# Optimization experiments

Measured on AMD Instinct MI355X. Metric: run time of the kernel, lower is better.

Reference implementation:

```python
import jax, jax.numpy as jnp
import numpy as np

E = 2048      # embedding_size
H = 16        # num_heads
D = 128       # head_dim
G = 4         # gqa_factor
KH = H // G   # kv heads
F = 8192      # up_proj_size
B, S = 2, 2048


def _layer_norm(x, g, b, eps=1e-5):
    mu = jnp.mean(x, axis=-1, keepdims=True)
    var = jnp.mean(jnp.square(x - mu), axis=-1, keepdims=True)
    return (x - mu) * jax.lax.rsqrt(var + eps) * g + b


def setup_inputs() -> dict:
    key = jax.random.key(0)
    ks = jax.random.split(key, 16)
    std = 0.02
    inp = {
        'x': jax.random.normal(ks[0], (B, S, E), dtype=jnp.float32),
        'ln1_g': jnp.ones((E,), jnp.float32),
        'ln1_b': jnp.zeros((E,), jnp.float32),
        'wq': jax.random.normal(ks[1], (E, H * D), jnp.float32) * std,
        'bq': jnp.zeros((H * D,), jnp.float32),
        'wk': jax.random.normal(ks[2], (E, KH * D), jnp.float32) * std,
        'bk': jnp.zeros((KH * D,), jnp.float32),
        'wv': jax.random.normal(ks[3], (E, KH * D), jnp.float32) * std,
        'bv': jnp.zeros((KH * D,), jnp.float32),
        'wo': jax.random.normal(ks[4], (H * D, E), jnp.float32) * std,
        'bo': jnp.zeros((E,), jnp.float32),
        'ln2_g': jnp.ones((E,), jnp.float32),
        'ln2_b': jnp.zeros((E,), jnp.float32),
        'wu': jax.random.normal(ks[5], (E, F), jnp.float32) * std,
        'bu': jnp.zeros((F,), jnp.float32),
        'wd': jax.random.normal(ks[6], (F, E), jnp.float32) * std,
        'bd': jnp.zeros((E,), jnp.float32),
    }
    return inp


def _block(x, ln1_g, ln1_b, wq, bq, wk, bk, wv, bv, wo, bo, ln2_g, ln2_b, wu, bu, wd, bd):
    b, s, e = x.shape
    # attention sub-block (use_cache=False, train_mode=False -> no dropout)
    x1 = _layer_norm(x, ln1_g, ln1_b)
    q = (x1 @ wq + bq).reshape(b, s, H, D).transpose(0, 2, 1, 3)       # (B,H,S,D)
    q = q.reshape(b, KH, G, s, D)                                       # (B,KH,G,S,D)
    k = (x1 @ wk + bk).reshape(b, s, KH, D).transpose(0, 2, 1, 3)      # (B,KH,S,D)
    v = (x1 @ wv + bv).reshape(b, s, KH, D).transpose(0, 2, 1, 3)      # (B,KH,S,D)
    scores = jnp.einsum('bkgsd,bktd->bkgst', q, k) / np.sqrt(D).astype(np.float32)
    causal = jnp.tril(jnp.ones((s, s), dtype=bool))                     # True = keep
    scores = jnp.where(causal, scores, -jnp.inf)
    att = jax.nn.softmax(scores, axis=-1)
    o = jnp.einsum('bkgst,bktd->bkgsd', att, v)                         # (B,KH,G,S,D)
    o = o.reshape(b, H, s, D).transpose(0, 2, 1, 3).reshape(b, s, H * D)
    x = x + (o @ wo + bo)
    # MLP sub-block
    x2 = _layer_norm(x, ln2_g, ln2_b)
    h = jax.nn.gelu(x2 @ wu + bu, approximate=False)
    x = x + (h @ wd + bd)
    return x


def reference(x, ln1_g, ln1_b, wq, bq, wk, bk, wv, bv, wo, bo, ln2_g, ln2_b, wu, bu, wd, bd):
    return _block(x, ln1_g, ln1_b, wq, bq, wk, bk, wv, bv, wo, bo, ln2_g, ln2_b, wu, bu, wd, bd)
```

## Files before the change

### kernel.cpp

```cpp
#include <hip/hip_runtime.h>
#include <hip/hip_bf16.h>
#include <cstdint>
#include <math.h>

typedef unsigned short u16;
using f32x4   = __attribute__((ext_vector_type(4))) float;
using short8  = __attribute__((ext_vector_type(8))) short;
using short4v = __attribute__((ext_vector_type(4))) short;

#define DEV static __device__ __forceinline__

DEV u16 f2bf(float f) {
  union { float f; unsigned u; } v; v.f = f;
  unsigned r = v.u + 0x7fffu + ((v.u >> 16) & 1u);
  return (u16)(r >> 16);
}

DEV f32x4 mfma_bf16(short8 a, short8 b, f32x4 c) {
  return __builtin_amdgcn_mfma_f32_16x16x32_bf16(a, b, c, 0, 0, 0);
}

DEV void gload16(const void* g, void* l) {
  __builtin_amdgcn_global_load_lds((const __attribute__((address_space(1))) void*)g,
                                   (__attribute__((address_space(3))) void*)l,
                                   16, 0, 0);
}

__global__ __launch_bounds__(256) void transpose_cvt(
    const float* __restrict__ in, u16* __restrict__ out, int K, int N)
{
  __shared__ float tile[32][33];
  const int n0 = blockIdx.x * 32, k0 = blockIdx.y * 32;
  const int c = threadIdx.x & 31, r = threadIdx.x >> 5;
#pragma unroll
  for (int i = 0; i < 4; i++) {
    const int row = r + i * 8;
    tile[row][c] = in[(size_t)(k0 + row) * N + n0 + c];
  }
  __syncthreads();
#pragma unroll
  for (int i = 0; i < 4; i++) {
    const int row = r + i * 8;
    out[(size_t)(n0 + row) * K + k0 + c] = f2bf(tile[c][row]);
  }
}

__global__ __launch_bounds__(256) void ln_kernel(
    const float* __restrict__ x, const float* __restrict__ g,
    const float* __restrict__ bt, u16* __restrict__ out)
{
  __shared__ float red1[4], red2[4];
  const int row = blockIdx.x;
  const int t = threadIdx.x;
  const int lane = t & 63, w = t >> 6;
  const float* xr = x + (size_t)row * 2048 + t * 8;
  float v[8];
  {
    const float4* p4 = (const float4*)xr;
    float4 a = p4[0], b = p4[1];
    v[0] = a.x; v[1] = a.y; v[2] = a.z; v[3] = a.w;
    v[4] = b.x; v[5] = b.y; v[6] = b.z; v[7] = b.w;
  }
  float s = 0.f;
#pragma unroll
  for (int j = 0; j < 8; j++) s += v[j];
#pragma unroll
  for (int m = 1; m < 64; m <<= 1) s += __shfl_xor(s, m);
  if (lane == 0) red1[w] = s;
  __syncthreads();
  const float mu = (red1[0] + red1[1] + red1[2] + red1[3]) * (1.f / 2048.f);
  float q = 0.f;
#pragma unroll
  for (int j = 0; j < 8; j++) { v[j] -= mu; q += v[j] * v[j]; }
#pragma unroll
  for (int m = 1; m < 64; m <<= 1) q += __shfl_xor(q, m);
  if (lane == 0) red2[w] = q;
  __syncthreads();
  const float rstd = rsqrtf((red2[0] + red2[1] + red2[2] + red2[3]) * (1.f / 2048.f) + 1e-5f);
  const float4* g4 = (const float4*)(g + t * 8);
  const float4* b4 = (const float4*)(bt + t * 8);
  float4 ga = g4[0], gb = g4[1], ba = b4[0], bb = b4[1];
  float gg[8] = {ga.x, ga.y, ga.z, ga.w, gb.x, gb.y, gb.z, gb.w};
  float bbv[8] = {ba.x, ba.y, ba.z, ba.w, bb.x, bb.y, bb.z, bb.w};
  short8 o;
#pragma unroll
  for (int j = 0; j < 8; j++) o[j] = (short)f2bf(v[j] * rstd * gg[j] + bbv[j]);
  *(short8*)&out[(size_t)row * 2048 + t * 8] = o;
}

template<int MODE, int N, int K>
__global__ void __launch_bounds__(256) gemm_bt(
    const u16* __restrict__ A, const u16* __restrict__ Bt,
    const float* __restrict__ bias,
    u16* __restrict__ out_bf)
{
  __shared__ u16 As[128 * 64];
  __shared__ u16 Bs[128 * 64];
  const int m0 = blockIdx.y * 128;
  const int n0 = blockIdx.x * 128;
  const int tid = threadIdx.x;
  const int lane = tid & 63, w = tid >> 6;
  const int wm = w >> 1, wn = w & 1;
  const int z = lane >> 4, l15 = lane & 15;

  f32x4 acc[4][4];
#pragma unroll
  for (int m = 0; m < 4; m++)
#pragma unroll
    for (int n = 0; n < 4; n++)
#pragma unroll
      for (int i = 0; i < 4; i++) acc[m][n][i] = 0.f;

  for (int k0 = 0; k0 < K; k0 += 64) {
#pragma unroll
    for (int j = 0; j < 4; j++) {
      const int seg = w * 4 + j;
      const int c = seg * 64 + lane;
      const int r = c >> 3;
      const int cc = (c & 7) ^ (r & 7);
      gload16(A + (size_t)(m0 + r) * K + k0 + cc * 8, &As[seg * 512]);
    }
#pragma unroll
    for (int j = 0; j < 4; j++) {
      const int seg = w * 4 + j;
      const int c = seg * 64 + lane;
      const int r = c >> 3;
      const int cc = (c & 7) ^ (r & 7);
      gload16(Bt + (size_t)(n0 + r) * K + k0 + cc * 8, &Bs[seg * 512]);
    }
    asm volatile("s_waitcnt vmcnt(0)" ::: "memory");
    __syncthreads();

#pragma unroll
    for (int kk = 0; kk < 2; kk++) {
      short8 af[4], bfr[4];
#pragma unroll
      for (int m = 0; m < 4; m++) {
        const int row = wm * 64 + m * 16 + l15;
        const int off = row * 64 + ((kk * 32 + z * 8) ^ ((row & 7) << 3));
        af[m] = *(const short8*)&As[off];
      }
#pragma unroll
      for (int n = 0; n < 4; n++) {
        const int row = wn * 64 + n * 16 + l15;
        const int off = row * 64 + ((kk * 32 + z * 8) ^ ((row & 7) << 3));
        bfr[n] = *(const short8*)&Bs[off];
      }
#pragma unroll
      for (int m = 0; m < 4; m++)
#pragma unroll
        for (int n = 0; n < 4; n++)
          acc[m][n] = mfma_bf16(af[m], bfr[n], acc[m][n]);
    }
    __syncthreads();
  }

#pragma unroll
  for (int m = 0; m < 4; m++) {
    const int row0 = m0 + wm * 64 + m * 16 + z * 4;
#pragma unroll
    for (int n = 0; n < 4; n++) {
      const int col = n0 + wn * 64 + n * 16 + l15;
      f32x4 v = acc[m][n];
      const float bb = bias[col];
      if constexpr (MODE == 1) {
#pragma unroll
        for (int i = 0; i < 4; i++)
          out_bf[(size_t)(row0 + i) * N + col] = f2bf(v[i] + bb);
      } else {
        const int bidx = row0 >> 11, sidx = row0 & 2047;
        const int kh = col >> 7, d = col & 127;
        short4v p;
#pragma unroll
        for (int i = 0; i < 4; i++) p[i] = (short)f2bf(v[i] + bb);
        *(short4v*)&out_bf[(size_t)((bidx * 4 + kh) * 128 + d) * 2048 + sidx] = p;
      }
    }
  }
}

template<int MODE, int BM, int N, int K>
__global__ void __launch_bounds__(512) gemm256(
    const u16* __restrict__ A, const u16* __restrict__ Bt,
    const float* __restrict__ bias, const float* __restrict__ resid,
    u16* __restrict__ out_bf, float* __restrict__ out_f)
{
  constexpr int BN = 256;
  constexpr int MREP = BM / 32;
  constexpr int LA = BM / 128;
  constexpr int L = LA + 2;
  constexpr int NT = K / 64;
  constexpr int NWG = (4096 / BM) * (N / BN);
  constexpr int CPX = NWG / 8;

  __shared__ u16 Al[2][2][BM * 32];
  __shared__ u16 Bl[2][2][BN * 32];

  const int bid = blockIdx.x;
  const int wg = (bid & 7) * CPX + (bid >> 3);
  const int bm = wg / (N / BN), bn = wg % (N / BN);
  const int m0 = bm * BM, n0 = bn * BN;
  const int tid = threadIdx.x, lane = tid & 63, w = tid >> 6;
  const int wm = w >> 2, wn = w & 3;
  const int z = lane >> 4, l15 = lane & 15;

  f32x4 acc[MREP][4];
#pragma unroll
  for (int m = 0; m < MREP; m++)
#pragma unroll
    for (int n = 0; n < 4; n++)
#pragma unroll
      for (int i = 0; i < 4; i++) acc[m][n][i] = 0.f;

  auto stage = [&](int tt, int kh) {
    const int buf = tt & 1;
    const int kc = tt * 64 + kh * 32;
#pragma unroll
    for (int j = 0; j < LA; j++) {
      const int gl = (w * LA + j) * 64 + lane;
      const int r = gl >> 2, gg = gl & 3;
      const int cg = gg ^ ((r >> 1) & 3);
      gload16(A + (size_t)(m0 + r) * K + kc + cg * 8, &Al[buf][kh][(w * LA + j) * 512]);
    }
#pragma unroll
    for (int j = 0; j < 2; j++) {
      const int gl = (w * 2 + j) * 64 + lane;
      const int r = gl >> 2, gg = gl & 3;
      const int cg = gg ^ ((r >> 1) & 3);
      gload16(Bt + (size_t)(n0 + r) * K + kc + cg * 8, &Bl[buf][kh][(w * 2 + j) * 512]);
    }
  };

  stage(0, 0); stage(0, 1); stage(1, 0); stage(1, 1);

  for (int t = 0; t < NT; t++) {
    const int cb = t & 1;
#pragma unroll
    for (int kh = 0; kh < 2; kh++) {
      if constexpr (L == 4) asm volatile("s_waitcnt vmcnt(4)" ::: "memory");
      else                  asm volatile("s_waitcnt vmcnt(3)" ::: "memory");
      __builtin_amdgcn_s_barrier();
      if (t + 1 < NT) stage(t + 1, kh);

      short8 af[MREP], bf[4];
#pragma unroll
      for (int m = 0; m < MREP; m++) {
        const int r = wm * (BM / 2) + m * 16 + l15;
        af[m] = *(const short8*)&Al[cb][kh][r * 32 + ((z ^ ((r >> 1) & 3)) * 8)];
      }
#pragma unroll
      for (int n = 0; n < 4; n++) {
        const int r = wn * 64 + n * 16 + l15;
        bf[n] = *(const short8*)&Bl[cb][kh][r * 32 + ((z ^ ((r >> 1) & 3)) * 8)];
      }
      __builtin_amdgcn_s_setprio(1);
#pragma unroll
      for (int m = 0; m < MREP; m++)
#pragma unroll
        for (int n = 0; n < 4; n++)
          acc[m][n] = mfma_bf16(af[m], bf[n], acc[m][n]);
      __builtin_amdgcn_s_setprio(0);
    }
  }

#pragma unroll
  for (int m = 0; m < MREP; m++) {
    const int row0 = m0 + wm * (BM / 2) + m * 16 + z * 4;
#pragma unroll
    for (int n = 0; n < 4; n++) {
      const int col = n0 + wn * 64 + n * 16 + l15;
      f32x4 v = acc[m][n];
      const float bb = bias[col];
      if constexpr (MODE == 0) {
#pragma unroll
        for (int i = 0; i < 4; i++)
          out_bf[(size_t)(row0 + i) * N + col] = f2bf((v[i] + bb) * 0.08838834764831845f);
      } else if constexpr (MODE == 3) {
#pragma unroll
        for (int i = 0; i < 4; i++) {
          const size_t idx = (size_t)(row0 + i) * N + col;
          out_f[idx] = v[i] + bb + resid[idx];
        }
      } else if constexpr (MODE == 4) {
#pragma unroll
        for (int i = 0; i < 4; i++) {
          const float xx = v[i] + bb;
          out_bf[(size_t)(row0 + i) * N + col] =
              f2bf(0.5f * xx * (1.f + erff(xx * 0.70710678118654752f)));
        }
      } else {
#pragma unroll
        for (int i = 0; i < 4; i++) {
          const size_t idx = (size_t)(row0 + i) * N + col;
          out_f[idx] = v[i] + bb + out_f[idx];
        }
      }
    }
  }
}

__global__ void __launch_bounds__(256) attn_kernel(
    const u16* __restrict__ qb, const u16* __restrict__ kb,
    const u16* __restrict__ vt, u16* __restrict__ ob)
{
  __shared__ u16 Kt[2][64 * 128];
  __shared__ u16 Vs[2][128 * 64];
  __shared__ u16 Pl[4 * 32 * 64];

  const int idx = blockIdx.x;
  const int xcd = idx & 7;
  const int u = (idx >> 3) & 31;
  const int half = idx >> 8;
  const int bh = xcd * 4 + (u & 3);
  const int qh = u >> 2;
  const int qt = half ? (15 - qh) : qh;

  const int b = bh >> 4, h = bh & 15, kh = h >> 2;
  const int q0 = qt * 128;
  const int tid = threadIdx.x, lane = tid & 63, w = tid >> 6;
  const int z = lane >> 4, l15 = lane & 15;
  const int qw0 = q0 + w * 32;
  const int ksw = (l15 & 7) << 3;

  short8 qf[2][4];
#pragma unroll
  for (int m = 0; m < 2; m++)
#pragma unroll
    for (int kk = 0; kk < 4; kk++)
      qf[m][kk] = *(const short8*)&qb[(size_t)(b * 2048 + qw0 + m * 16 + l15) * 2048 +
                                      h * 128 + kk * 32 + z * 8];

  f32x4 oacc[2][8];
#pragma unroll
  for (int m = 0; m < 2; m++)
#pragma unroll
    for (int n = 0; n < 8; n++)
#pragma unroll
      for (int i = 0; i < 4; i++) oacc[m][n][i] = 0.f;
  float mst[2][4], lst[2][4];
#pragma unroll
  for (int m = 0; m < 2; m++)
#pragma unroll
    for (int i = 0; i < 4; i++) { mst[m][i] = -1e30f; lst[m][i] = 0.f; }

  auto STAGE = [&](int tt, int bufsel) {
    const int kv0s = tt * 64;
#pragma unroll
    for (int j = 0; j < 4; j++) {
      const int seg = w * 4 + j;
      const int c = seg * 64 + lane;
      const int r = c >> 4;
      const int cc = (c & 15) ^ (r & 7);
      gload16(kb + (size_t)(b * 2048 + kv0s + r) * 512 + kh * 128 + cc * 8,
              &Kt[bufsel][seg * 512]);
    }
#pragma unroll
    for (int j = 0; j < 4; j++) {
      const int seg = w * 4 + j;
      const int c = seg * 64 + lane;
      const int d = c >> 3;
      const int cc = (c & 7) ^ (d & 7);
      gload16(vt + (size_t)((b * 4 + kh) * 128 + d) * 2048 + kv0s + cc * 8,
              &Vs[bufsel][seg * 512]);
    }
  };

  const int ntiles = q0 / 64 + 2;

  STAGE(0, 0);
  asm volatile("s_waitcnt vmcnt(0)" ::: "memory");
  __syncthreads();

  for (int t = 0; t < ntiles; t++) {
    const int cur = t & 1;
    if (t + 1 < ntiles) STAGE(t + 1, cur ^ 1);

    const int kv0 = t * 64;
    if (kv0 <= qw0 + 31) {
      f32x4 sf[2][4];
#pragma unroll
      for (int m = 0; m < 2; m++)
#pragma unroll
        for (int n = 0; n < 4; n++)
#pragma unroll
          for (int i = 0; i < 4; i++) sf[m][n][i] = 0.f;

      __builtin_amdgcn_s_setprio(1);
#pragma unroll
      for (int kk = 0; kk < 4; kk++) {
        short8 kfr[4];
#pragma unroll
        for (int n = 0; n < 4; n++) {
          const int row = n * 16 + l15;
          kfr[n] = *(const short8*)&Kt[cur][row * 128 + ((kk * 32 + z * 8) ^ ksw)];
        }
#pragma unroll
        for (int m = 0; m < 2; m++)
#pragma unroll
          for (int n = 0; n < 4; n++)
            sf[m][n] = mfma_bf16(qf[m][kk], kfr[n], sf[m][n]);
      }
      __builtin_amdgcn_s_setprio(0);

      u16* Pw = &Pl[w * 2048];
      const bool edge = (kv0 + 63 > qw0);
#pragma unroll
      for (int m = 0; m < 2; m++) {
#pragma unroll
        for (int i = 0; i < 4; i++) {
          const int rq = qw0 + m * 16 + z * 4 + i;
          if (edge) {
#pragma unroll
            for (int n = 0; n < 4; n++)
              if (kv0 + n * 16 + l15 > rq) sf[m][n][i] = -1e30f;
          }
          float mx = fmaxf(fmaxf(sf[m][0][i], sf[m][1][i]), fmaxf(sf[m][2][i], sf[m][3][i]));
          mx = fmaxf(mx, __shfl_xor(mx, 1));
          mx = fmaxf(mx, __shfl_xor(mx, 2));
          mx = fmaxf(mx, __shfl_xor(mx, 4));
          mx = fmaxf(mx, __shfl_xor(mx, 8));
          const bool grow = mx > mst[m][i];
          const float mn = grow ? mx : mst[m][i];
          float rs = 0.f;
#pragma unroll
          for (int n = 0; n < 4; n++) {
            const float p = __expf(sf[m][n][i] - mn);
            sf[m][n][i] = p;
            rs += p;
          }
          rs += __shfl_xor(rs, 1);
          rs += __shfl_xor(rs, 2);
          rs += __shfl_xor(rs, 4);
          rs += __shfl_xor(rs, 8);
          if (grow) {
            const float al = __expf(mst[m][i] - mx);
            mst[m][i] = mx;
            lst[m][i] = lst[m][i] * al + rs;
#pragma unroll
            for (int n = 0; n < 8; n++) oacc[m][n][i] *= al;
          } else {
            lst[m][i] += rs;
          }
          const int prow = m * 16 + z * 4 + i;
          const int psw = ((z * 4 + i) & 7) << 3;
#pragma unroll
          for (int n = 0; n < 4; n++)
            Pw[prow * 64 + ((n * 16 + l15) ^ psw)] = f2bf(sf[m][n][i]);
        }
      }

      __builtin_amdgcn_s_setprio(1);
#pragma unroll
      for (int kk = 0; kk < 2; kk++) {
        short8 af[2], vf[8];
#pragma unroll
        for (int m = 0; m < 2; m++) {
          const int row = m * 16 + l15;
          af[m] = *(const short8*)&Pw[row * 64 + ((kk * 32 + z * 8) ^ ksw)];
        }
#pragma unroll
        for (int n = 0; n < 8; n++) {
          const int row = n * 16 + l15;
          vf[n] = *(const short8*)&Vs[cur][row * 64 + ((kk * 32 + z * 8) ^ ksw)];
        }
#pragma unroll
        for (int m = 0; m < 2; m++)
#pragma unroll
          for (int n = 0; n < 8; n++)
            oacc[m][n] = mfma_bf16(af[m], vf[n], oacc[m][n]);
      }
      __builtin_amdgcn_s_setprio(0);
    }

    asm volatile("s_waitcnt vmcnt(0)" ::: "memory");
    __syncthreads();
  }

#pragma unroll
  for (int m = 0; m < 2; m++)
#pragma unroll
    for (int i = 0; i < 4; i++) {
      const float inv = 1.0f / lst[m][i];
      const int rq = qw0 + m * 16 + z * 4 + i;
      u16* orow = &ob[(size_t)(b * 2048 + rq) * 2048 + h * 128];
#pragma unroll
      for (int n = 0; n < 8; n++)
        orow[n * 16 + l15] = f2bf(oacc[m][n][i] * inv);
    }
}

extern "C" void kernel_launch(void* const* d_in, const int* in_sizes, int n_in,
                              void* d_out, int out_size, void* d_ws, size_t ws_size,
                              hipStream_t stream) {
  (void)in_sizes; (void)n_in; (void)out_size; (void)ws_size;
  const float* x     = (const float*)d_in[0];
  const float* ln1_g = (const float*)d_in[1];
  const float* ln1_b = (const float*)d_in[2];
  const float* wq    = (const float*)d_in[3];
  const float* bq    = (const float*)d_in[4];
  const float* wk    = (const float*)d_in[5];
  const float* bk    = (const float*)d_in[6];
  const float* wv    = (const float*)d_in[7];
  const float* bv    = (const float*)d_in[8];
  const float* wo    = (const float*)d_in[9];
  const float* bo    = (const float*)d_in[10];
  const float* ln2_g = (const float*)d_in[11];
  const float* ln2_b = (const float*)d_in[12];
  const float* wu    = (const float*)d_in[13];
  const float* bu    = (const float*)d_in[14];
  const float* wd    = (const float*)d_in[15];
  const float* bd    = (const float*)d_in[16];
  float* out = (float*)d_out;

  char* p = (char*)d_ws;
  u16* wqT = (u16*)p; p += (size_t)2048 * 2048 * 2;
  u16* wkT = (u16*)p; p += (size_t)512 * 2048 * 2;
  u16* wvT = (u16*)p; p += (size_t)512 * 2048 * 2;
  u16* woT = (u16*)p; p += (size_t)2048 * 2048 * 2;
  u16* wuT = (u16*)p; p += (size_t)8192 * 2048 * 2;
  u16* wdT = (u16*)p; p += (size_t)2048 * 8192 * 2;
  u16* x1  = (u16*)p; p += (size_t)4096 * 2048 * 2;
  u16* qbuf= (u16*)p; p += (size_t)4096 * 2048 * 2;
  u16* kbuf= (u16*)p; p += (size_t)4096 * 512 * 2;
  u16* vtb = (u16*)p; p += (size_t)4096 * 512 * 2;
  u16* hb  = (u16*)p; p += (size_t)4096 * 8192 * 2;
  u16* ob  = x1;
  u16* x2  = qbuf;

  transpose_cvt<<<dim3(64, 64),  256, 0, stream>>>(wq, wqT, 2048, 2048);
  transpose_cvt<<<dim3(16, 64),  256, 0, stream>>>(wk, wkT, 2048, 512);
  transpose_cvt<<<dim3(16, 64),  256, 0, stream>>>(wv, wvT, 2048, 512);
  transpose_cvt<<<dim3(64, 64),  256, 0, stream>>>(wo, woT, 2048, 2048);
  transpose_cvt<<<dim3(256, 64), 256, 0, stream>>>(wu, wuT, 2048, 8192);
  transpose_cvt<<<dim3(64, 256), 256, 0, stream>>>(wd, wdT, 8192, 2048);

  ln_kernel<<<4096, 256, 0, stream>>>(x, ln1_g, ln1_b, x1);

  gemm256<0, 128, 2048, 2048><<<256, 512, 0, stream>>>(x1, wqT, bq, nullptr, qbuf, nullptr);
  gemm_bt<1, 512, 2048><<<dim3(4, 32), 256, 0, stream>>>(x1, wkT, bk, kbuf);
  gemm_bt<2, 512, 2048><<<dim3(4, 32), 256, 0, stream>>>(x1, wvT, bv, vtb);

  attn_kernel<<<512, 256, 0, stream>>>(qbuf, kbuf, vtb, ob);

  gemm256<3, 128, 2048, 2048><<<256, 512, 0, stream>>>(ob, woT, bo, x, nullptr, out);

  ln_kernel<<<4096, 256, 0, stream>>>(out, ln2_g, ln2_b, x2);

  gemm256<4, 256, 8192, 2048><<<512, 512, 0, stream>>>(x2, wuT, bu, nullptr, hb, nullptr);
  gemm256<5, 128, 2048, 8192><<<256, 512, 0, stream>>>(hb, wdT, bd, nullptr, nullptr, out);
}
```

Measured before the change: 836.9 us.

## Restructure GEMM mainloop into a 4-slot ring with 3-deep prefetch

Replaces the double-buffered two-half-tile pipeline in the shared GEMM kernel with a 4-slot ring of 32-wide K slices, issuing loads three phases ahead and waiting on per-phase vmcnt values. It also precomputes the swizzled LDS and global address offsets once per thread instead of per load. The goal is to hide more global-load latency and cut address arithmetic. In exchange it adds a second barrier per phase, and the same LDS footprint is now split into smaller slices.

```diff
diff --git a/kernel.cpp b/kernel.cpp
--- a/kernel.cpp
+++ b/kernel.cpp
@@ -188,13 +188,12 @@
   constexpr int BN = 256;
   constexpr int MREP = BM / 32;
   constexpr int LA = BM / 128;
-  constexpr int L = LA + 2;
-  constexpr int NT = K / 64;
+  constexpr int P = K / 32;
   constexpr int NWG = (4096 / BM) * (N / BN);
   constexpr int CPX = NWG / 8;
 
-  __shared__ u16 Al[2][2][BM * 32];
-  __shared__ u16 Bl[2][2][BN * 32];
+  __shared__ u16 Al[4][BM * 32];
+  __shared__ u16 Bl[4][BN * 32];
 
   const int bid = blockIdx.x;
   const int wg = (bid & 7) * CPX + (bid >> 3);
@@ -203,6 +202,11 @@
   const int tid = threadIdx.x, lane = tid & 63, w = tid >> 6;
   const int wm = w >> 2, wn = w & 3;
   const int z = lane >> 4, l15 = lane & 15;
+  const int wmBase = wm * (BM / 2);
+  const int wnBase = wn * 64;
+  const int koff = (z ^ ((l15 >> 1) & 3)) * 8;
+  const int col8 = ((lane & 3) ^ ((lane >> 3) & 3)) * 8;
+  const int srow = lane >> 2;
 
   f32x4 acc[MREP][4];
 #pragma unroll
@@ -212,63 +216,71 @@
 #pragma unroll
       for (int i = 0; i < 4; i++) acc[m][n][i] = 0.f;
 
-  auto stage = [&](int tt, int kh) {
-    const int buf = tt & 1;
-    const int kc = tt * 64 + kh * 32;
+  auto stage = [&](int g) {
+    const int sl = g & 3;
+    const int kc = g * 32;
 #pragma unroll
     for (int j = 0; j < LA; j++) {
-      const int gl = (w * LA + j) * 64 + lane;
-      const int r = gl >> 2, gg = gl & 3;
-      const int cg = gg ^ ((r >> 1) & 3);
-      gload16(A + (size_t)(m0 + r) * K + kc + cg * 8, &Al[buf][kh][(w * LA + j) * 512]);
+      const int sweep = w * LA + j;
+      gload16(A + (size_t)(m0 + sweep * 16 + srow) * K + kc + col8, &Al[sl][sweep * 512]);
     }
 #pragma unroll
     for (int j = 0; j < 2; j++) {
-      const int gl = (w * 2 + j) * 64 + lane;
-      const int r = gl >> 2, gg = gl & 3;
-      const int cg = gg ^ ((r >> 1) & 3);
-      gload16(Bt + (size_t)(n0 + r) * K + kc + cg * 8, &Bl[buf][kh][(w * 2 + j) * 512]);
+      const int sweep = w * 2 + j;
+      gload16(Bt + (size_t)(n0 + sweep * 16 + srow) * K + kc + col8, &Bl[sl][sweep * 512]);
     }
   };
 
-  stage(0, 0); stage(0, 1); stage(1, 0); stage(1, 1);
-
-  for (int t = 0; t < NT; t++) {
-    const int cb = t & 1;
-#pragma unroll
-    for (int kh = 0; kh < 2; kh++) {
-      if constexpr (L == 4) asm volatile("s_waitcnt vmcnt(4)" ::: "memory");
-      else                  asm volatile("s_waitcnt vmcnt(3)" ::: "memory");
-      __builtin_amdgcn_s_barrier();
-      if (t + 1 < NT) stage(t + 1, kh);
-
-      short8 af[MREP], bf[4];
-#pragma unroll
-      for (int m = 0; m < MREP; m++) {
-        const int r = wm * (BM / 2) + m * 16 + l15;
-        af[m] = *(const short8*)&Al[cb][kh][r * 32 + ((z ^ ((r >> 1) & 3)) * 8)];
-      }
-#pragma unroll
-      for (int n = 0; n < 4; n++) {
-        const int r = wn * 64 + n * 16 + l15;
-        bf[n] = *(const short8*)&Bl[cb][kh][r * 32 + ((z ^ ((r >> 1) & 3)) * 8)];
-      }
-      __builtin_amdgcn_s_setprio(1);
-#pragma unroll
-      for (int m = 0; m < MREP; m++)
-#pragma unroll
-        for (int n = 0; n < 4; n++)
-          acc[m][n] = mfma_bf16(af[m], bf[n], acc[m][n]);
-      __builtin_amdgcn_s_setprio(0);
-    }
-  }
+#define PHASE(pp, VMSTR, DOSTAGE)                                              \
+  do {                                                                         \
+    asm volatile("s_waitcnt " VMSTR ::: "memory");                             \
+    __builtin_amdgcn_s_barrier();                                              \
+    asm volatile("" ::: "memory");                                             \
+    if (DOSTAGE) stage((pp) + 3);                                              \
+    const int sl_ = (pp) & 3;                                                  \
+    const u16* Ab_ = &Al[sl_][0];                                              \
+    const u16* Bb_ = &Bl[sl_][0];                                              \
+    short8 af_[MREP], bf_[4];                                                  \
+    _Pragma("unroll")                                                          \
+    for (int m = 0; m < MREP; m++)                                             \
+      af_[m] = *(const short8*)&Ab_[(wmBase + m * 16 + l15) * 32 + koff];      \
+    _Pragma("unroll")                                                          \
+    for (int n = 0; n < 4; n++)                                                \
+      bf_[n] = *(const short8*)&Bb_[(wnBase + n * 16 + l15) * 32 + koff];      \
+    asm volatile("s_waitcnt lgkmcnt(0)" ::: "memory");                         \
+    __builtin_amdgcn_sched_barrier(0);                                         \
+    __builtin_amdgcn_s_setprio(1);                                             \
+    _Pragma("unroll")                                                          \
+    for (int m = 0; m < MREP; m++)                                             \
+      _Pragma("unroll")                                                        \
+      for (int n = 0; n < 4; n++)                                              \
+        acc[m][n] = mfma_bf16(af_[m], bf_[n], acc[m][n]);                      \
+    __builtin_amdgcn_s_setprio(0);                                             \
+    asm volatile("" ::: "memory");                                             \
+    __builtin_amdgcn_s_barrier();                                              \
+  } while (0)
+
+  stage(0); stage(1); stage(2);
+
+  if constexpr (LA == 2) {
+    for (int p = 0; p < P - 3; p++) PHASE(p, "vmcnt(8)", true);
+    PHASE(P - 3, "vmcnt(8)", false);
+    PHASE(P - 2, "vmcnt(4)", false);
+    PHASE(P - 1, "vmcnt(0)", false);
+  } else {
+    for (int p = 0; p < P - 3; p++) PHASE(p, "vmcnt(6)", true);
+    PHASE(P - 3, "vmcnt(6)", false);
+    PHASE(P - 2, "vmcnt(3)", false);
+    PHASE(P - 1, "vmcnt(0)", false);
+  }
+#undef PHASE
 
 #pragma unroll
   for (int m = 0; m < MREP; m++) {
-    const int row0 = m0 + wm * (BM / 2) + m * 16 + z * 4;
+    const int row0 = m0 + wmBase + m * 16 + z * 4;
 #pragma unroll
     for (int n = 0; n < 4; n++) {
-      const int col = n0 + wn * 64 + n * 16 + l15;
+      const int col = n0 + wnBase + n * 16 + l15;
       f32x4 v = acc[m][n];
       const float bb = bias[col];
       if constexpr (MODE == 0) {
```

Result: slower. 867.1 us (+3.6%).

## Replace 512-thread 256-wide GEMM with 128x128 double-buffered 256-thread kernel

Applied to the files above, without the earlier changes.

Swaps the large-tile gemm256 kernel (BM up to 256, BN 256, 8 waves, split-k-half staging with partial vmcnt waits) for a simpler 128x128 tile, 4-wave kernel. The new kernel double-buffers full 64-wide K slices and waits on all loads plus a block-wide sync each iteration. It also uses an XOR-8 LDS swizzle. The smaller tiles launch more workgroups and may raise occupancy, but they lower per-tile data reuse and drop the finer-grained load/compute overlap.

```diff
diff --git a/kernel.cpp b/kernel.cpp
--- a/kernel.cpp
+++ b/kernel.cpp
@@ -179,93 +179,95 @@
   }
 }
 
-template<int MODE, int BM, int N, int K>
-__global__ void __launch_bounds__(512) gemm256(
+template<int MODE, int N, int K>
+__global__ void __launch_bounds__(256) gemm_db(
     const u16* __restrict__ A, const u16* __restrict__ Bt,
     const float* __restrict__ bias, const float* __restrict__ resid,
     u16* __restrict__ out_bf, float* __restrict__ out_f)
 {
-  constexpr int BN = 256;
-  constexpr int MREP = BM / 32;
-  constexpr int LA = BM / 128;
-  constexpr int L = LA + 2;
+  __shared__ u16 As[2][128 * 64];
+  __shared__ u16 Bs[2][128 * 64];
+  constexpr int TN = N / 128;
+  constexpr int NWG = 32 * TN;
+  constexpr int CPX = NWG / 8;
   constexpr int NT = K / 64;
-  constexpr int NWG = (4096 / BM) * (N / BN);
-  constexpr int CPX = NWG / 8;
-
-  __shared__ u16 Al[2][2][BM * 32];
-  __shared__ u16 Bl[2][2][BN * 32];
 
   const int bid = blockIdx.x;
   const int wg = (bid & 7) * CPX + (bid >> 3);
-  const int bm = wg / (N / BN), bn = wg % (N / BN);
-  const int m0 = bm * BM, n0 = bn * BN;
-  const int tid = threadIdx.x, lane = tid & 63, w = tid >> 6;
-  const int wm = w >> 2, wn = w & 3;
+  const int m0 = (wg / TN) * 128;
+  const int n0 = (wg % TN) * 128;
+  const int tid = threadIdx.x;
+  const int lane = tid & 63, w = tid >> 6;
+  const int wm = w >> 1, wn = w & 1;
   const int z = lane >> 4, l15 = lane & 15;
 
-  f32x4 acc[MREP][4];
-#pragma unroll
-  for (int m = 0; m < MREP; m++)
+  f32x4 acc[4][4];
+#pragma unroll
+  for (int m = 0; m < 4; m++)
 #pragma unroll
     for (int n = 0; n < 4; n++)
 #pragma unroll
       for (int i = 0; i < 4; i++) acc[m][n][i] = 0.f;
 
-  auto stage = [&](int tt, int kh) {
-    const int buf = tt & 1;
-    const int kc = tt * 64 + kh * 32;
-#pragma unroll
-    for (int j = 0; j < LA; j++) {
-      const int gl = (w * LA + j) * 64 + lane;
-      const int r = gl >> 2, gg = gl & 3;
-      const int cg = gg ^ ((r >> 1) & 3);
-      gload16(A + (size_t)(m0 + r) * K + kc + cg * 8, &Al[buf][kh][(w * LA + j) * 512]);
-    }
-#pragma unroll
-    for (int j = 0; j < 2; j++) {
-      const int gl = (w * 2 + j) * 64 + lane;
-      const int r = gl >> 2, gg = gl & 3;
-      const int cg = gg ^ ((r >> 1) & 3);
-      gload16(Bt + (size_t)(n0 + r) * K + kc + cg * 8, &Bl[buf][kh][(w * 2 + j) * 512]);
+  auto stage = [&](int k0, int buf) {
+#pragma unroll
+    for (int j = 0; j < 4; j++) {
+      const int seg = w * 4 + j;
+      const int c = seg * 64 + lane;
+      const int r = c >> 3;
+      const int cc = (c & 7) ^ (r & 7);
+      gload16(A + (size_t)(m0 + r) * K + k0 + cc * 8, &As[buf][seg * 512]);
+    }
+#pragma unroll
+    for (int j = 0; j < 4; j++) {
+      const int seg = w * 4 + j;
+      const int c = seg * 64 + lane;
+      const int r = c >> 3;
+      const int cc = (c & 7) ^ (r & 7);
+      gload16(Bt + (size_t)(n0 + r) * K + k0 + cc * 8, &Bs[buf][seg * 512]);
     }
   };
 
-  stage(0, 0); stage(0, 1); stage(1, 0); stage(1, 1);
-
+  stage(0, 0);
+  asm volatile("s_waitcnt vmcnt(0)" ::: "memory");
+  __syncthreads();
+
+  int cur = 0;
   for (int t = 0; t < NT; t++) {
-    const int cb = t & 1;
-#pragma unroll
-    for (int kh = 0; kh < 2; kh++) {
-      if constexpr (L == 4) asm volatile("s_waitcnt vmcnt(4)" ::: "memory");
-      else                  asm volatile("s_waitcnt vmcnt(3)" ::: "memory");
-      __builtin_amdgcn_s_barrier();
-      if (t + 1 < NT) stage(t + 1, kh);
-
-      short8 af[MREP], bf[4];
-#pragma unroll
-      for (int m = 0; m < MREP; m++) {
-        const int r = wm * (BM / 2) + m * 16 + l15;
-        af[m] = *(const short8*)&Al[cb][kh][r * 32 + ((z ^ ((r >> 1) & 3)) * 8)];
+    if (t + 1 < NT) stage((t + 1) * 64, cur ^ 1);
+
+#pragma unroll
+    for (int kk = 0; kk < 2; kk++) {
+      short8 af[4], bfr[4];
+#pragma unroll
+      for (int m = 0; m < 4; m++) {
+        const int row = wm * 64 + m * 16 + l15;
+        const int off = row * 64 + ((kk * 32 + z * 8) ^ ((row & 7) << 3));
+        af[m] = *(const short8*)&As[cur][off];
       }
 #pragma unroll
       for (int n = 0; n < 4; n++) {
-        const int r = wn * 64 + n * 16 + l15;
-        bf[n] = *(const short8*)&Bl[cb][kh][r * 32 + ((z ^ ((r >> 1) & 3)) * 8)];
+        const int row = wn * 64 + n * 16 + l15;
+        const int off = row * 64 + ((kk * 32 + z * 8) ^ ((row & 7) << 3));
+        bfr[n] = *(const short8*)&Bs[cur][off];
       }
       __builtin_amdgcn_s_setprio(1);
 #pragma unroll
-      for (int m = 0; m < MREP; m++)
+      for (int m = 0; m < 4; m++)
 #pragma unroll
         for (int n = 0; n < 4; n++)
-          acc[m][n] = mfma_bf16(af[m], bf[n], acc[m][n]);
+          acc[m][n] = mfma_bf16(af[m], bfr[n], acc[m][n]);
       __builtin_amdgcn_s_setprio(0);
     }
-  }
-
-#pragma unroll
-  for (int m = 0; m < MREP; m++) {
-    const int row0 = m0 + wm * (BM / 2) + m * 16 + z * 4;
+
+    asm volatile("s_waitcnt vmcnt(0)" ::: "memory");
+    __syncthreads();
+    cur ^= 1;
+  }
+
+#pragma unroll
+  for (int m = 0; m < 4; m++) {
+    const int row0 = m0 + wm * 64 + m * 16 + z * 4;
 #pragma unroll
     for (int n = 0; n < 4; n++) {
       const int col = n0 + wn * 64 + n * 16 + l15;
@@ -536,16 +538,16 @@
 
   ln_kernel<<<4096, 256, 0, stream>>>(x, ln1_g, ln1_b, x1);
 
-  gemm256<0, 128, 2048, 2048><<<256, 512, 0, stream>>>(x1, wqT, bq, nullptr, qbuf, nullptr);
+  gemm_db<0, 2048, 2048><<<512, 256, 0, stream>>>(x1, wqT, bq, nullptr, qbuf, nullptr);
   gemm_bt<1, 512, 2048><<<dim3(4, 32), 256, 0, stream>>>(x1, wkT, bk, kbuf);
   gemm_bt<2, 512, 2048><<<dim3(4, 32), 256, 0, stream>>>(x1, wvT, bv, vtb);
 
   attn_kernel<<<512, 256, 0, stream>>>(qbuf, kbuf, vtb, ob);
 
-  gemm256<3, 128, 2048, 2048><<<256, 512, 0, stream>>>(ob, woT, bo, x, nullptr, out);
+  gemm_db<3, 2048, 2048><<<512, 256, 0, stream>>>(ob, woT, bo, x, nullptr, out);
 
   ln_kernel<<<4096, 256, 0, stream>>>(out, ln2_g, ln2_b, x2);
 
-  gemm256<4, 256, 8192, 2048><<<512, 512, 0, stream>>>(x2, wuT, bu, nullptr, hb, nullptr);
-  gemm256<5, 128, 2048, 8192><<<256, 512, 0, stream>>>(hb, wdT, bd, nullptr, nullptr, out);
-}
+  gemm_db<4, 8192, 2048><<<2048, 256, 0, stream>>>(x2, wuT, bu, nullptr, hb, nullptr);
+  gemm_db<5, 2048, 8192><<<512, 256, 0, stream>>>(hb, wdT, bd, nullptr, nullptr, out);
+}
```

Result: faster. 745.2 us (-11.0%).
